# Kernel tuning notes

Hardware: AMD Instinct MI355X
Metric: run time of the kernel (lower is better)

Reference implementation:

```python
import jax, jax.numpy as jnp
import numpy as np

B, S = 1, 2048
D = 4096          # hidden_size
H, HK, DH = 32, 8, 128  # num_heads, num_kv_heads, head_dim
THETA = 10000.0


def setup_inputs() -> dict:
    key = jax.random.key(0)
    k0, k1, k2, k3, k4 = jax.random.split(key, 5)
    std = 0.02
    return {
        "position_ids": jnp.broadcast_to(jnp.arange(S, dtype=jnp.int32), (B, S)),
        "hidden_states": jax.random.normal(k0, (B, S, D), jnp.float32),
        "Wq": (jax.random.normal(k1, (D, H * DH), jnp.float32) * std),
        "Wk": (jax.random.normal(k2, (D, HK * DH), jnp.float32) * std),
        "Wv": (jax.random.normal(k3, (D, HK * DH), jnp.float32) * std),
        "Wo": (jax.random.normal(k4, (H * DH, D), jnp.float32) * std),
    }


def _rope(x, pos):
    """Neox-style rotary embedding over the full head_dim. x: [B,S,h,DH]."""
    half = DH // 2
    inv_freq = 1.0 / (THETA ** (jnp.arange(half, dtype=jnp.float32) * 2.0 / DH))
    ang = pos[..., None].astype(jnp.float32) * inv_freq          # [B,S,half]
    cos = jnp.cos(ang)[:, :, None, :]
    sin = jnp.sin(ang)[:, :, None, :]
    x1, x2 = x[..., :half], x[..., half:]
    return jnp.concatenate([x1 * cos - x2 * sin, x2 * cos + x1 * sin], axis=-1)


def reference(position_ids, hidden_states, Wq, Wk, Wv, Wo):
    q = (hidden_states @ Wq).reshape(B, S, H, DH)
    k = (hidden_states @ Wk).reshape(B, S, HK, DH)
    v = (hidden_states @ Wv).reshape(B, S, HK, DH)
    q = _rope(q, position_ids)
    k = _rope(k, position_ids)

    G = H // HK  # query heads per kv head (GQA)
    qg = q.reshape(B, S, HK, G, DH)
    scale = jnp.float32(DH) ** -0.5
    scores = jnp.einsum('bqhgd,bkhd->bhgqk', qg, k) * scale      # [B,HK,G,S,S]
    causal = jnp.tril(jnp.ones((S, S), dtype=bool))
    scores = jnp.where(causal, scores, jnp.finfo(scores.dtype).min)
    p = jax.nn.softmax(scores, axis=-1)
    out = jnp.einsum('bhgqk,bkhd->bqhgd', p, v).reshape(B, S, H * DH)
    return out @ Wo
```

## Files before the change

### kernel.cpp

```cpp
#include <hip/hip_runtime.h>

typedef unsigned short u16;
typedef short bf16x8 __attribute__((ext_vector_type(8)));
typedef float f32x4 __attribute__((ext_vector_type(4)));

#define GLB __attribute__((address_space(1)))
#define LDSAS __attribute__((address_space(3)))

constexpr int S = 2048, D = 4096, NH = 32, NHK = 8, DHD = 128;
constexpr int NQKV = 6144;

__device__ __forceinline__ u16 f2b(float f) {
    union { float f; unsigned u; } v; v.f = f;
    return (u16)((v.u + 0x7fffu + ((v.u >> 16) & 1u)) >> 16);
}
__device__ __forceinline__ float b2f(u16 b) {
    union { unsigned u; float f; } v; v.u = ((unsigned)b) << 16;
    return v.f;
}
__device__ __forceinline__ void gload16(const void* g, void* l) {
    __builtin_amdgcn_global_load_lds((const GLB unsigned int*)g,
                                     (LDSAS unsigned int*)l, 16, 0, 0);
}
#if __has_builtin(__builtin_amdgcn_exp2f)
__device__ __forceinline__ float exp2fast(float x) { return __builtin_amdgcn_exp2f(x); }
#else
__device__ __forceinline__ float exp2fast(float x) { return __expf(0.6931471805599453f * x); }
#endif

__device__ __forceinline__ void sincos_big(float ang, float* sn, float* cs) {
#if __has_builtin(__builtin_amdgcn_sinf) && __has_builtin(__builtin_amdgcn_cosf)
    float rev = ang * 0.15915494309189535f;
    rev = rev - floorf(rev);
    *sn = __builtin_amdgcn_sinf(rev);
    *cs = __builtin_amdgcn_cosf(rev);
#else
    *sn = sinf(ang);
    *cs = cosf(ang);
#endif
}

__global__ __launch_bounds__(256) void cvt_x(const float* __restrict__ in,
                                             u16* __restrict__ out, int n8) {
    int i = blockIdx.x * 256 + threadIdx.x;
    if (i >= n8) return;
    const float4* p = (const float4*)in + (size_t)i * 2;
    float4 a = p[0], b = p[1];
    uint4 o;
    o.x = f2b(a.x) | ((unsigned)f2b(a.y) << 16);
    o.y = f2b(a.z) | ((unsigned)f2b(a.w) << 16);
    o.z = f2b(b.x) | ((unsigned)f2b(b.y) << 16);
    o.w = f2b(b.z) | ((unsigned)f2b(b.w) << 16);
    *(uint4*)(out + (size_t)i * 8) = o;
}

__global__ __launch_bounds__(256) void tconv(const float* __restrict__ in,
                                             u16* __restrict__ out, int R, int C) {
    __shared__ float t[64][65];
    int r0 = blockIdx.y * 64, c0 = blockIdx.x * 64;
    int tx = threadIdx.x & 63, ty = threadIdx.x >> 6;
#pragma unroll
    for (int i = 0; i < 64; i += 4)
        t[ty + i][tx] = in[(size_t)(r0 + ty + i) * C + c0 + tx];
    __syncthreads();
#pragma unroll
    for (int i = 0; i < 64; i += 4)
        out[(size_t)(c0 + ty + i) * R + r0 + tx] = f2b(t[tx][ty + i]);
}

__global__ __launch_bounds__(256) void vtrans(const u16* __restrict__ QKV,
                                              u16* __restrict__ Vt) {
    __shared__ u16 t[64][65];
    int hk = blockIdx.z;
    int s0 = blockIdx.x * 64, d0 = blockIdx.y * 64;
    int tx = threadIdx.x & 63, ty = threadIdx.x >> 6;
#pragma unroll
    for (int i = 0; i < 64; i += 4)
        t[ty + i][tx] = QKV[(size_t)(s0 + ty + i) * NQKV + 5120 + hk * 128 + d0 + tx];
    __syncthreads();
#pragma unroll
    for (int i = 0; i < 64; i += 4)
        Vt[(size_t)hk * (128 * 2048) + (size_t)(d0 + ty + i) * 2048 + s0 + tx] = t[tx][ty + i];
}

template <int NHEADS>
__global__ __launch_bounds__(256) void rope2(u16* __restrict__ T,
                                             const int* __restrict__ pos, float scale) {
    int idx = blockIdx.x * 256 + threadIdx.x;
    int d = idx & 63;
    int h = (idx >> 6) & (NHEADS - 1);
    int s = idx >> (6 + (NHEADS == 32 ? 5 : 3));
    float p = (float)pos[s];
    float inv = __expf(-(float)d * 0.14391156531310576f);
    float ang = p * inv;
    float sn, cs;
    sincos_big(ang, &sn, &cs);
    size_t base = (size_t)s * NQKV + h * 128 + d;
    float x1 = b2f(T[base]), x2 = b2f(T[base + 64]);
    T[base]      = f2b((x1 * cs - x2 * sn) * scale);
    T[base + 64] = f2b((x2 * cs + x1 * sn) * scale);
}

template <bool BF16OUT>
__global__ __launch_bounds__(256) void gemmS(const u16* __restrict__ A,
                                             const u16* __restrict__ Bt,
                                             void* __restrict__ Cout,
                                             int N, int K, int nbx) {
    __shared__ u16 Asm[128 * 64];
    __shared__ u16 Bsm[128 * 64];
    const int cpx = (int)gridDim.x >> 3;
    const int b = ((int)blockIdx.x & 7) * cpx + ((int)blockIdx.x >> 3);
    const int by = b / nbx, bx = b - by * nbx;
    const int m0 = by * 128, n0 = bx * 128;
    const int tid = threadIdx.x, lane = tid & 63, wave = tid >> 6;
    const int l15 = lane & 15, l4 = lane >> 4;
    const int wm = wave >> 1, wn = wave & 1;
    f32x4 acc[4][4] = {};

    for (int k0 = 0; k0 < K; k0 += 64) {
        __syncthreads();
#pragma unroll
        for (int u = 0; u < 4; ++u) {
            int s = u * 256 + tid;
            int row = s >> 3, cs = (s & 7) ^ (row & 7);
            gload16(A  + (size_t)(m0 + row) * K + k0 + cs * 8, Asm + s * 8);
            gload16(Bt + (size_t)(n0 + row) * K + k0 + cs * 8, Bsm + s * 8);
        }
        __syncthreads();
        bf16x8 af[4][2], bf[4][2];
#pragma unroll
        for (int i = 0; i < 4; ++i)
#pragma unroll
            for (int kk = 0; kk < 2; ++kk) {
                int row = wm * 64 + i * 16 + l15;
                int cc = (kk * 4 + l4) ^ (row & 7);
                af[i][kk] = *(const bf16x8*)(Asm + row * 64 + cc * 8);
            }
#pragma unroll
        for (int j = 0; j < 4; ++j)
#pragma unroll
            for (int kk = 0; kk < 2; ++kk) {
                int row = wn * 64 + j * 16 + l15;
                int cc = (kk * 4 + l4) ^ (row & 7);
                bf[j][kk] = *(const bf16x8*)(Bsm + row * 64 + cc * 8);
            }
#pragma unroll
        for (int i = 0; i < 4; ++i)
#pragma unroll
            for (int j = 0; j < 4; ++j)
#pragma unroll
                for (int kk = 0; kk < 2; ++kk)
                    acc[i][j] = __builtin_amdgcn_mfma_f32_16x16x32_bf16(af[i][kk], bf[j][kk], acc[i][j], 0, 0, 0);
    }
#pragma unroll
    for (int i = 0; i < 4; ++i)
#pragma unroll
        for (int j = 0; j < 4; ++j) {
            int col  = n0 + wn * 64 + j * 16 + l15;
            int rowb = m0 + wm * 64 + i * 16 + l4 * 4;
#pragma unroll
            for (int r = 0; r < 4; ++r) {
                if (BF16OUT)
                    ((u16*)Cout)[(size_t)(rowb + r) * N + col] = f2b(acc[i][j][r]);
                else
                    ((float*)Cout)[(size_t)(rowb + r) * N + col] = acc[i][j][r];
            }
        }
}

__global__ __launch_bounds__(256) void attn3(const u16* __restrict__ QKV,
                                             const u16* __restrict__ Vt,
                                             u16* __restrict__ O) {
    __shared__ u16 Ksm[2][64 * 128];
    __shared__ u16 Vsm[2][128 * 64];
    __shared__ u16 Psm[4][16 * 64];
    const int orig = blockIdx.x;
    const int swz = (orig & 7) * 64 + (orig >> 3);
    const int h = swz >> 4, p = swz & 15;
    const int hk = h >> 2;
    const int tid = threadIdx.x, wave = tid >> 6, lane = tid & 63;
    const int l15 = lane & 15, l4 = lane >> 4;
    const u16* Qp = QKV + h * 128;
    const u16* Kp = QKV + 4096 + hk * 128;
    const u16* Vp = Vt + (size_t)hk * (128 * 2048);

    auto stage = [&](int kb, int b) {
#pragma unroll
        for (int it = 0; it < 4; ++it) {
            int L = it * 256 + tid;
            int krow = L >> 4, kslot = L & 15;
            int kcs = (kslot & 8) | ((kslot ^ krow) & 7);
            gload16(Kp + (size_t)(kb * 64 + krow) * NQKV + kcs * 8, &Ksm[b][L * 8]);
            int vrow = L >> 3, vslot = L & 7;
            int vcs = (vslot ^ vrow) & 7;
            gload16(Vp + (size_t)vrow * 2048 + kb * 64 + vcs * 8, &Vsm[b][L * 8]);
        }
    };

#pragma unroll 1
    for (int pass = 0; pass < 2; ++pass) {
        const int qt = pass ? p : 31 - p;
        const int qr0 = qt * 64 + wave * 16;
        const int nkb = qt + 1;

        bf16x8 qf[4];
        {
            const u16* qrow = Qp + (size_t)(qr0 + l15) * NQKV;
#pragma unroll
            for (int c = 0; c < 4; ++c)
                qf[c] = *(const bf16x8*)(qrow + c * 32 + l4 * 8);
        }
        float mrow[4], lsum[4];
#pragma unroll
        for (int r = 0; r < 4; ++r) { mrow[r] = -1e30f; lsum[r] = 0.f; }
        f32x4 o[8] = {};

        stage(0, 0);
#pragma unroll 1
        for (int kb = 0; kb < nkb; ++kb) {
            const int cur = kb & 1;
            if (kb + 1 < nkb) {
                stage(kb + 1, cur ^ 1);
                asm volatile("s_waitcnt vmcnt(8)" ::: "memory");
            } else {
                asm volatile("s_waitcnt vmcnt(0)" ::: "memory");
            }
            __builtin_amdgcn_s_barrier();

            if (kb * 64 <= qr0 + 15) {
                const u16* Kb_ = Ksm[cur];
                const u16* Vb_ = Vsm[cur];
                const bool diag = (kb * 64 + 63 > qr0);
                f32x4 sc[4] = {};
#pragma unroll
                for (int f = 0; f < 4; ++f) {
                    const int kv = f * 16 + l15;
#pragma unroll
                    for (int c = 0; c < 4; ++c) {
                        int cd = c * 4 + l4;
                        int cpos = (cd & 8) | ((cd ^ kv) & 7);
                        bf16x8 kf = *(const bf16x8*)(Kb_ + kv * 128 + cpos * 8);
                        sc[f] = __builtin_amdgcn_mfma_f32_16x16x32_bf16(qf[c], kf, sc[f], 0, 0, 0);
                    }
                }
                if (diag) {
#pragma unroll
                    for (int f = 0; f < 4; ++f) {
                        int col = kb * 64 + f * 16 + l15;
#pragma unroll
                        for (int r = 0; r < 4; ++r) {
                            int row = qr0 + l4 * 4 + r;
                            if (col > row) sc[f][r] = -1e30f;
                        }
                    }
                }
                float bm[4];
#pragma unroll
                for (int r = 0; r < 4; ++r)
                    bm[r] = fmaxf(fmaxf(sc[0][r], sc[1][r]), fmaxf(sc[2][r], sc[3][r]));
                bool need = false;
#pragma unroll
                for (int r = 0; r < 4; ++r) need = need || (bm[r] > mrow[r] + 8.0f);
                if (__any((int)need)) {
#pragma unroll
                    for (int msk = 1; msk < 16; msk <<= 1)
#pragma unroll
                        for (int r = 0; r < 4; ++r) bm[r] = fmaxf(bm[r], __shfl_xor(bm[r], msk));
                    float al[4];
#pragma unroll
                    for (int r = 0; r < 4; ++r) {
                        float mn = fmaxf(mrow[r], bm[r]);
                        al[r] = exp2fast(mrow[r] - mn);
                        mrow[r] = mn;
                        lsum[r] *= al[r];
                    }
#pragma unroll
                    for (int n = 0; n < 8; ++n)
#pragma unroll
                        for (int r = 0; r < 4; ++r) o[n][r] *= al[r];
                }
#pragma unroll
                for (int f = 0; f < 4; ++f) {
#pragma unroll
                    for (int r = 0; r < 4; ++r) {
                        float pw = exp2fast(sc[f][r] - mrow[r]);
                        lsum[r] += pw;
                        int q = l4 * 4 + r;
                        int kvc = f * 2 + (l15 >> 3);
                        int slot = (kvc ^ q) & 7;
                        Psm[wave][q * 64 + slot * 8 + (l15 & 7)] = f2b(pw);
                    }
                }

                asm volatile("s_waitcnt lgkmcnt(0)" ::: "memory");
                bf16x8 pf[2];
#pragma unroll
                for (int c = 0; c < 2; ++c) {
                    int chc = c * 4 + l4;
                    int slot = (chc ^ l15) & 7;
                    pf[c] = *(const bf16x8*)(&Psm[wave][l15 * 64 + slot * 8]);
                }
#pragma unroll
                for (int n = 0; n < 8; ++n) {
                    int d = n * 16 + l15;
                    bf16x8 vf[2];
#pragma unroll
                    for (int c = 0; c < 2; ++c) {
                        int ch = c * 4 + l4;
                        int slot = (ch ^ d) & 7;
                        vf[c] = *(const bf16x8*)(Vb_ + d * 64 + slot * 8);
                    }
#pragma unroll
                    for (int c = 0; c < 2; ++c)
                        o[n] = __builtin_amdgcn_mfma_f32_16x16x32_bf16(pf[c], vf[c], o[n], 0, 0, 0);
                }
            }
            asm volatile("s_waitcnt lgkmcnt(0)" ::: "memory");
            __builtin_amdgcn_s_barrier();
        }

#pragma unroll
        for (int msk = 1; msk < 16; msk <<= 1)
#pragma unroll
            for (int r = 0; r < 4; ++r) lsum[r] += __shfl_xor(lsum[r], msk);
        float inv[4];
#pragma unroll
        for (int r = 0; r < 4; ++r) inv[r] = 1.0f / lsum[r];
#pragma unroll
        for (int n = 0; n < 8; ++n)
#pragma unroll
            for (int r = 0; r < 4; ++r) {
                int row = qr0 + l4 * 4 + r;
                O[(size_t)row * 4096 + h * 128 + n * 16 + l15] = f2b(o[n][r] * inv[r]);
            }
    }
}

extern "C" void kernel_launch(void* const* d_in, const int* in_sizes, int n_in,
                              void* d_out, int out_size, void* d_ws, size_t ws_size,
                              hipStream_t stream) {
    const int*   pos = (const int*)d_in[0];
    const float* X   = (const float*)d_in[1];
    const float* Wq  = (const float*)d_in[2];
    const float* Wk  = (const float*)d_in[3];
    const float* Wv  = (const float*)d_in[4];
    const float* Wo  = (const float*)d_in[5];
    float* out = (float*)d_out;

    char* w = (char*)d_ws;
    u16* Xb    = (u16*)(w + 0);
    u16* Wqkvt = (u16*)(w + 16777216);
    u16* Wot   = (u16*)(w + 67108864);
    u16* QKV   = (u16*)(w + 100663296);
    u16* Vtb   = (u16*)(w + 125829120);
    u16* Ob    = (u16*)(w + 130023424);

    const float SC2 = 0.08838834764831845f * 1.4426950408889634f;

    cvt_x<<<4096, 256, 0, stream>>>(X, Xb, S * D / 8);
    tconv<<<dim3(64, 64), 256, 0, stream>>>(Wq, Wqkvt, 4096, 4096);
    tconv<<<dim3(16, 64), 256, 0, stream>>>(Wk, Wqkvt + (size_t)4096 * 4096, 4096, 1024);
    tconv<<<dim3(16, 64), 256, 0, stream>>>(Wv, Wqkvt + (size_t)5120 * 4096, 4096, 1024);
    tconv<<<dim3(64, 64), 256, 0, stream>>>(Wo, Wot, 4096, 4096);

    gemmS<true><<<768, 256, 0, stream>>>(Xb, Wqkvt, QKV, NQKV, 4096, 48);

    rope2<32><<<16384, 256, 0, stream>>>(QKV, pos, SC2);
    rope2<8><<<4096, 256, 0, stream>>>(QKV + 4096, pos, 1.0f);

    vtrans<<<dim3(32, 2, 8), 256, 0, stream>>>(QKV, Vtb);

    attn3<<<512, 256, 0, stream>>>(QKV, Vtb, Ob);

    gemmS<false><<<512, 256, 0, stream>>>(Ob, Wot, out, 4096, 4096, 32);
}
```

Before: 350.8 us.

## Split-K the output projection GEMM into two bf16 partials plus a reduction

The output projection GEMM now splits K into two halves and runs 1024 blocks instead of 512, so more workgroups are available to fill the CUs. Each half writes bf16 partials into reused workspace, and a new elementwise kernel adds them into the fp32 output. The extra partial traffic, the extra launch, and rounding the partials to bf16 (which costs accuracy) are traded for the added parallelism.

```diff
diff --git a/kernel.cpp b/kernel.cpp
--- a/kernel.cpp
+++ b/kernel.cpp
@@ -52,6 +52,25 @@
     o.z = f2b(b.x) | ((unsigned)f2b(b.y) << 16);
     o.w = f2b(b.z) | ((unsigned)f2b(b.w) << 16);
     *(uint4*)(out + (size_t)i * 8) = o;
+}
+
+__global__ __launch_bounds__(256) void red2(const u16* __restrict__ P,
+                                            float* __restrict__ out, int n8) {
+    int i = blockIdx.x * 256 + threadIdx.x;
+    if (i >= n8) return;
+    uint4 a = *(const uint4*)(P + (size_t)i * 8);
+    uint4 b = *(const uint4*)(P + (size_t)(8388608) + (size_t)i * 8);
+    float4 o0, o1;
+    o0.x = b2f((u16)a.x) + b2f((u16)b.x);
+    o0.y = b2f((u16)(a.x >> 16)) + b2f((u16)(b.x >> 16));
+    o0.z = b2f((u16)a.y) + b2f((u16)b.y);
+    o0.w = b2f((u16)(a.y >> 16)) + b2f((u16)(b.y >> 16));
+    o1.x = b2f((u16)a.z) + b2f((u16)b.z);
+    o1.y = b2f((u16)(a.z >> 16)) + b2f((u16)(b.z >> 16));
+    o1.z = b2f((u16)a.w) + b2f((u16)b.w);
+    o1.w = b2f((u16)(a.w >> 16)) + b2f((u16)(b.w >> 16));
+    float4* q = (float4*)(out + (size_t)i * 8);
+    q[0] = o0; q[1] = o1;
 }
 
 __global__ __launch_bounds__(256) void tconv(const float* __restrict__ in,
@@ -105,26 +124,31 @@
 __global__ __launch_bounds__(256) void gemmS(const u16* __restrict__ A,
                                              const u16* __restrict__ Bt,
                                              void* __restrict__ Cout,
-                                             int N, int K, int nbx) {
+                                             int N, int Kstride, int nbx,
+                                             int kch, int klen) {
     __shared__ u16 Asm[128 * 64];
     __shared__ u16 Bsm[128 * 64];
     const int cpx = (int)gridDim.x >> 3;
     const int b = ((int)blockIdx.x & 7) * cpx + ((int)blockIdx.x >> 3);
-    const int by = b / nbx, bx = b - by * nbx;
+    const int per = (int)gridDim.x / kch;
+    const int ks = b / per, ib = b - ks * per;
+    const int by = ib / nbx, bx = ib - by * nbx;
     const int m0 = by * 128, n0 = bx * 128;
+    const int kbeg = ks * klen;
+    const size_t obase = (size_t)ks * 2048 * N;
     const int tid = threadIdx.x, lane = tid & 63, wave = tid >> 6;
     const int l15 = lane & 15, l4 = lane >> 4;
     const int wm = wave >> 1, wn = wave & 1;
     f32x4 acc[4][4] = {};
 
-    for (int k0 = 0; k0 < K; k0 += 64) {
+    for (int k0 = kbeg; k0 < kbeg + klen; k0 += 64) {
         __syncthreads();
 #pragma unroll
         for (int u = 0; u < 4; ++u) {
             int s = u * 256 + tid;
             int row = s >> 3, cs = (s & 7) ^ (row & 7);
-            gload16(A  + (size_t)(m0 + row) * K + k0 + cs * 8, Asm + s * 8);
-            gload16(Bt + (size_t)(n0 + row) * K + k0 + cs * 8, Bsm + s * 8);
+            gload16(A  + (size_t)(m0 + row) * Kstride + k0 + cs * 8, Asm + s * 8);
+            gload16(Bt + (size_t)(n0 + row) * Kstride + k0 + cs * 8, Bsm + s * 8);
         }
         __syncthreads();
         bf16x8 af[4][2], bf[4][2];
@@ -161,9 +185,9 @@
 #pragma unroll
             for (int r = 0; r < 4; ++r) {
                 if (BF16OUT)
-                    ((u16*)Cout)[(size_t)(rowb + r) * N + col] = f2b(acc[i][j][r]);
+                    ((u16*)Cout)[obase + (size_t)(rowb + r) * N + col] = f2b(acc[i][j][r]);
                 else
-                    ((float*)Cout)[(size_t)(rowb + r) * N + col] = acc[i][j][r];
+                    ((float*)Cout)[obase + (size_t)(rowb + r) * N + col] = acc[i][j][r];
             }
         }
 }
@@ -354,6 +378,7 @@
     u16* QKV   = (u16*)(w + 100663296);
     u16* Vtb   = (u16*)(w + 125829120);
     u16* Ob    = (u16*)(w + 130023424);
+    u16* Pp    = (u16*)(w + 0);
 
     const float SC2 = 0.08838834764831845f * 1.4426950408889634f;
 
@@ -363,7 +388,7 @@
     tconv<<<dim3(16, 64), 256, 0, stream>>>(Wv, Wqkvt + (size_t)5120 * 4096, 4096, 1024);
     tconv<<<dim3(64, 64), 256, 0, stream>>>(Wo, Wot, 4096, 4096);
 
-    gemmS<true><<<768, 256, 0, stream>>>(Xb, Wqkvt, QKV, NQKV, 4096, 48);
+    gemmS<true><<<768, 256, 0, stream>>>(Xb, Wqkvt, QKV, NQKV, 4096, 48, 1, 4096);
 
     rope2<32><<<16384, 256, 0, stream>>>(QKV, pos, SC2);
     rope2<8><<<4096, 256, 0, stream>>>(QKV + 4096, pos, 1.0f);
@@ -372,5 +397,6 @@
 
     attn3<<<512, 256, 0, stream>>>(QKV, Vtb, Ob);
 
-    gemmS<false><<<512, 256, 0, stream>>>(Ob, Wot, out, 4096, 4096, 32);
-}
+    gemmS<true><<<1024, 256, 0, stream>>>(Ob, Wot, Pp, 4096, 4096, 32, 2, 2048);
+    red2<<<4096, 256, 0, stream>>>(Pp, out, 1048576);
+}
```

Result: slower. 377.7 us (+7.7%).
